# Performance work log

Measured on AMD Instinct MI355X. Metric: run time of the kernel, lower is better.

## Reference

```python
import jax, jax.numpy as jnp
import numpy as np
from jax import lax

IN_CH = 256
OUT_CH = 256
INTER = IN_CH // 2
KERNEL = 3


def setup_inputs() -> dict:
    key = jax.random.key(0)
    ks = jax.random.split(key, 6)
    B, C, H, W = 8, IN_CH, 128, 128
    x = jax.random.normal(ks[0], (B, C, H, W), dtype=jnp.float32)
    s = 1.0 / np.sqrt(C)
    Wq = jax.random.normal(ks[1], (INTER, C), dtype=jnp.float32) * s
    Wk = jax.random.normal(ks[2], (INTER, C), dtype=jnp.float32) * s
    Wv = jax.random.normal(ks[3], (INTER, C), dtype=jnp.float32) * s
    w1d = jax.random.normal(ks[4], (KERNEL,), dtype=jnp.float32) * (1.0 / np.sqrt(KERNEL))
    Wc = jax.random.normal(ks[5], (OUT_CH, INTER, 3, 3), dtype=jnp.float32) * (1.0 / np.sqrt(INTER * 9))
    return {"x": x, "Wq": Wq, "Wk": Wk, "Wv": Wv, "w1d": w1d, "Wc": Wc}


def reference(x, Wq, Wk, Wv, w1d, Wc):
    B, C, H, W = x.shape
    inter = Wq.shape[0]
    Hs, Ws = H // 4, W // 4  # 1x1 conv, stride 4, pad 0 == spatial subsample
    xs = x[:, :, ::4, ::4]  # [B, C, Hs, Ws]
    q = jnp.einsum('oc,bchw->bohw', Wq, xs).reshape(B, inter, Hs * Ws)  # [B, inter, N]
    k = jnp.einsum('oc,bchw->bohw', Wk, xs).reshape(B, inter, Hs * Ws)
    v = jnp.einsum('oc,bchw->bohw', Wv, xs).reshape(B, inter, Hs * Ws)
    # gate = softmax(Q^T K) over last dim, shape [B, N, N]
    scores = jnp.einsum('bcn,bcm->bnm', q, k)
    gate = jax.nn.softmax(scores, axis=-1)
    # gated value: [B, inter, N] -> [B, inter, Hs, Ws]
    gv = jnp.einsum('bnm,bcm->bcn', gate, v).reshape(B, inter, Hs, Ws)
    # ECA channel gating: global avg pool -> conv1d over channel dim -> sigmoid
    ca = gv.mean(axis=(2, 3))  # [B, inter]
    ca = lax.conv_general_dilated(
        ca[:, None, :],                     # [B, 1, inter]
        w1d[None, None, :],                 # [1, 1, K]
        window_strides=(1,), padding=[((KERNEL - 1) // 2,) * 2],
        dimension_numbers=('NCH', 'OIH', 'NCH'))
    ca = jax.nn.sigmoid(ca)[:, 0, :, None, None]  # [B, inter, 1, 1]
    out = gv * ca
    out = lax.conv_general_dilated(
        out, Wc, window_strides=(1, 1), padding='SAME',
        dimension_numbers=('NCHW', 'OIHW', 'NCHW'))
    return out, gate, ca
```

## Files before the change

kernel.cpp:

```cpp
#include <hip/hip_runtime.h>
#include <math.h>

#define B_   8
#define C_   256
#define CI_  128
#define N_   1024
#define HW_  32
#define CO_  256

typedef __bf16 v8bf __attribute__((ext_vector_type(8)));
typedef float  f32x4 __attribute__((ext_vector_type(4)));
typedef unsigned short ushort_t;

__device__ __forceinline__ unsigned short f2bf_rne(float f) {
    unsigned int u = __float_as_uint(f);
    unsigned int r = u + 0x7FFF + ((u >> 16) & 1);
    return (unsigned short)(r >> 16);
}
__device__ __forceinline__ float bf2f(unsigned short h) {
    return __uint_as_float(((unsigned int)h) << 16);
}
__device__ __forceinline__ v8bf ld8(const ushort_t* p) {
    return *(const v8bf*)p;
}

__global__ __launch_bounds__(256) void prep_all_kernel(
    const float* __restrict__ x,
    const float* __restrict__ Wc,
    const float* __restrict__ Wq, const float* __restrict__ Wk,
    const float* __restrict__ Wv,
    ushort_t* __restrict__ Whi, ushort_t* __restrict__ Wlo,
    ushort_t* __restrict__ Wp_hi, ushort_t* __restrict__ Wp_lo,
    ushort_t* __restrict__ xs_hi, ushort_t* __restrict__ xs_lo,
    float* __restrict__ meanb)
{
    __shared__ ushort_t lh[32 * 72];
    __shared__ ushort_t ll[32 * 72];
    const int bx = blockIdx.x;
    const int tid = threadIdx.x;

    if (bx < 1152) {
        if (bx == 0) {
            *(float4*)&meanb[tid * 4] = make_float4(0.f, 0.f, 0.f, 0.f);
        }
        int idx = bx * 256 + tid;
        int o = idx / 1152;
        int r = idx - o * 1152;
        int ci = r / 9;
        int tap = r - ci * 9;
        float v = Wc[idx];
        unsigned short h = f2bf_rne(v);
        unsigned short l = f2bf_rne(v - bf2f(h));
        int didx = o * 1152 + tap * 128 + ci;
        Whi[didx] = h; Wlo[didx] = l;
    } else if (bx < 1536) {
        int j = (bx - 1152) * 256 + tid;
        int o = j >> 8, c = j & 255;
        float v = (o < 128) ? Wq[o * 256 + c]
                : (o < 256) ? Wk[(o - 128) * 256 + c]
                            : Wv[(o - 256) * 256 + c];
        unsigned short h = f2bf_rne(v);
        unsigned short l = f2bf_rne(v - bf2f(h));
        Wp_hi[j] = h; Wp_lo[j] = l;
    } else {
        const int bx2 = bx - 1536;
        const int cq = bx2 & 3;
        const int h  = (bx2 >> 2) & 31;
        const int b  = bx2 >> 7;
        const int w = tid & 31, cg = tid >> 5;
        float v[8];
        #pragma unroll
        for (int i = 0; i < 8; ++i) {
            int c = cq * 64 + i * 8 + cg;
            v[i] = x[((size_t)(b * C_ + c) * 128 + h * 4) * 128 + w * 4];
        }
        #pragma unroll
        for (int i = 0; i < 8; ++i) {
            int cl = i * 8 + cg;
            unsigned short hi = f2bf_rne(v[i]);
            unsigned short lo = f2bf_rne(v[i] - bf2f(hi));
            lh[w * 72 + cl] = hi;
            ll[w * 72 + cl] = lo;
        }
        __syncthreads();
        const int ww = tid >> 3, cs = tid & 7;
        size_t dst = ((size_t)(b * N_) + h * 32 + ww) * 256 + cq * 64 + cs * 8;
        *(uint4*)&xs_hi[dst] = *(uint4*)&lh[ww * 72 + cs * 8];
        *(uint4*)&xs_lo[dst] = *(uint4*)&ll[ww * 72 + cs * 8];
    }
}

__global__ __launch_bounds__(256) void proj_mfma_kernel(
    const ushort_t* __restrict__ Wp_hi, const ushort_t* __restrict__ Wp_lo,
    const ushort_t* __restrict__ xs_hi, const ushort_t* __restrict__ xs_lo,
    ushort_t* __restrict__ qt_hi, ushort_t* __restrict__ qt_lo,
    ushort_t* __restrict__ kt_hi, ushort_t* __restrict__ kt_lo,
    ushort_t* __restrict__ vB_hi, ushort_t* __restrict__ vB_lo)
{
    const int lin = blockIdx.x + 16 * (blockIdx.y + 6 * blockIdx.z);
    const int b    = lin & 7;
    const int rest = lin >> 3;
    const int n0 = (rest & 15) * 64;
    const int o0 = (rest >> 4) * 64;
    const int tid = threadIdx.x;
    const int l = tid & 63, wv = tid >> 6;
    const int wy = wv >> 1, wx = wv & 1;
    const int ln = l & 15, quad = l >> 4;

    const ushort_t* Ah_p[2]; const ushort_t* Al_p[2];
    const ushort_t* Bh_p[2]; const ushort_t* Bl_p[2];
    #pragma unroll
    for (int i = 0; i < 2; ++i) {
        size_t off = (size_t)(o0 + wy * 32 + i * 16 + ln) * 256 + quad * 8;
        Ah_p[i] = Wp_hi + off; Al_p[i] = Wp_lo + off;
    }
    #pragma unroll
    for (int j = 0; j < 2; ++j) {
        size_t off = ((size_t)(b * N_) + n0 + wx * 32 + j * 16 + ln) * 256 + quad * 8;
        Bh_p[j] = xs_hi + off; Bl_p[j] = xs_lo + off;
    }

    f32x4 acc[2][2];
    #pragma unroll
    for (int i = 0; i < 2; ++i)
        #pragma unroll
        for (int j = 0; j < 2; ++j) acc[i][j] = (f32x4){0.f,0.f,0.f,0.f};

    if (o0 < 256) {
        #pragma unroll 4
        for (int k0 = 0; k0 < 256; k0 += 32) {
            v8bf Ah[2], Al[2], Bh[2], Bl[2];
            #pragma unroll
            for (int i = 0; i < 2; ++i) { Ah[i] = ld8(Ah_p[i] + k0); Al[i] = ld8(Al_p[i] + k0); }
            #pragma unroll
            for (int j = 0; j < 2; ++j) { Bh[j] = ld8(Bh_p[j] + k0); Bl[j] = ld8(Bl_p[j] + k0); }
            __builtin_amdgcn_s_setprio(1);
            #pragma unroll
            for (int i = 0; i < 2; ++i)
                #pragma unroll
                for (int j = 0; j < 2; ++j) {
                    acc[i][j] = __builtin_amdgcn_mfma_f32_16x16x32_bf16(Ah[i], Bh[j], acc[i][j], 0, 0, 0);
                    acc[i][j] = __builtin_amdgcn_mfma_f32_16x16x32_bf16(Ah[i], Bl[j], acc[i][j], 0, 0, 0);
                    acc[i][j] = __builtin_amdgcn_mfma_f32_16x16x32_bf16(Al[i], Bh[j], acc[i][j], 0, 0, 0);
                }
            __builtin_amdgcn_s_setprio(0);
        }
        ushort_t* th = (o0 < 128) ? qt_hi : kt_hi;
        ushort_t* tl = (o0 < 128) ? qt_lo : kt_lo;
        const int ob = o0 & 127;
        #pragma unroll
        for (int i = 0; i < 2; ++i)
            #pragma unroll
            for (int j = 0; j < 2; ++j) {
                int oo = ob + wy * 32 + i * 16 + quad * 4;
                int n  = n0 + wx * 32 + j * 16 + ln;
                unsigned int h01 = 0, h23 = 0, l01 = 0, l23 = 0;
                #pragma unroll
                for (int r = 0; r < 4; ++r) {
                    float f = acc[i][j][r];
                    unsigned short hh = f2bf_rne(f);
                    unsigned short lo = f2bf_rne(f - bf2f(hh));
                    if (r < 2) { h01 |= ((unsigned)hh) << (16 * r); l01 |= ((unsigned)lo) << (16 * r); }
                    else       { h23 |= ((unsigned)hh) << (16 * (r - 2)); l23 |= ((unsigned)lo) << (16 * (r - 2)); }
                }
                size_t off = ((size_t)(b * N_) + n) * 128 + oo;
                *(uint2*)&th[off] = make_uint2(h01, h23);
                *(uint2*)&tl[off] = make_uint2(l01, l23);
            }
    } else {
        #pragma unroll 4
        for (int k0 = 0; k0 < 256; k0 += 32) {
            v8bf Ah[2], Al[2], Bh[2], Bl[2];
            #pragma unroll
            for (int i = 0; i < 2; ++i) { Ah[i] = ld8(Ah_p[i] + k0); Al[i] = ld8(Al_p[i] + k0); }
            #pragma unroll
            for (int j = 0; j < 2; ++j) { Bh[j] = ld8(Bh_p[j] + k0); Bl[j] = ld8(Bl_p[j] + k0); }
            __builtin_amdgcn_s_setprio(1);
            #pragma unroll
            for (int j = 0; j < 2; ++j)
                #pragma unroll
                for (int i = 0; i < 2; ++i) {
                    acc[j][i] = __builtin_amdgcn_mfma_f32_16x16x32_bf16(Bh[j], Ah[i], acc[j][i], 0, 0, 0);
                    acc[j][i] = __builtin_amdgcn_mfma_f32_16x16x32_bf16(Bh[j], Al[i], acc[j][i], 0, 0, 0);
                    acc[j][i] = __builtin_amdgcn_mfma_f32_16x16x32_bf16(Bl[j], Ah[i], acc[j][i], 0, 0, 0);
                }
            __builtin_amdgcn_s_setprio(0);
        }
        const int mhi = (n0 >> 5) + wx;
        #pragma unroll
        for (int j = 0; j < 2; ++j)
            #pragma unroll
            for (int i = 0; i < 2; ++i) {
                int c   = (o0 - 256) + wy * 32 + i * 16 + ln;
                int mlo = j * 16 + quad * 4;
                unsigned int h01 = 0, h23 = 0, l01 = 0, l23 = 0;
                #pragma unroll
                for (int r = 0; r < 4; ++r) {
                    float f = acc[j][i][r];
                    unsigned short hh = f2bf_rne(f);
                    unsigned short lo = f2bf_rne(f - bf2f(hh));
                    if (r < 2) { h01 |= ((unsigned)hh) << (16 * r); l01 |= ((unsigned)lo) << (16 * r); }
                    else       { h23 |= ((unsigned)hh) << (16 * (r - 2)); l23 |= ((unsigned)lo) << (16 * (r - 2)); }
                }
                size_t off = (((size_t)b * 32 + mhi) * 128 + c) * 32 + mlo;
                *(uint2*)&vB_hi[off] = make_uint2(h01, h23);
                *(uint2*)&vB_lo[off] = make_uint2(l01, l23);
            }
    }
}

__global__ __launch_bounds__(512, 2) void attn_fused_kernel(
    const ushort_t* __restrict__ qt_hi, const ushort_t* __restrict__ qt_lo,
    const ushort_t* __restrict__ kt_hi, const ushort_t* __restrict__ kt_lo,
    const ushort_t* __restrict__ vB_hi, const ushort_t* __restrict__ vB_lo,
    float* __restrict__ gate, float* __restrict__ gv, float* __restrict__ meanb)
{
    __shared__ __align__(16) char gsm[65536];
    __shared__ float redA[8][32];
    __shared__ float redB[8][32];

    const int lin = blockIdx.x + 32 * blockIdx.y;
    const int b  = lin & 7;
    const int n0 = (lin >> 3) * 32;
    const int tid = threadIdx.x;
    const int l = tid & 63, w = tid >> 6;
    const int ln = l & 15, quad = l >> 4;
    const int Mw = w * 128;

    const ushort_t* qb_h = qt_hi + ((size_t)(b * N_) + n0) * 128;
    const ushort_t* qb_l = qt_lo + ((size_t)(b * N_) + n0) * 128;
    const ushort_t* kb_h = kt_hi + (size_t)(b * N_) * 128;
    const ushort_t* kb_l = kt_lo + (size_t)(b * N_) * 128;

    f32x4 acc[2][8];
    #pragma unroll
    for (int nt = 0; nt < 2; ++nt)
        #pragma unroll
        for (int mt = 0; mt < 8; ++mt) acc[nt][mt] = (f32x4){0.f,0.f,0.f,0.f};

    #pragma unroll
    for (int c0 = 0; c0 < 128; c0 += 32) {
        v8bf Ah[2], Al[2];
        #pragma unroll
        for (int nt = 0; nt < 2; ++nt) {
            size_t aoff = (size_t)(nt * 16 + ln) * 128 + c0 + quad * 8;
            Ah[nt] = ld8(qb_h + aoff); Al[nt] = ld8(qb_l + aoff);
        }
        #pragma unroll
        for (int mt = 0; mt < 8; ++mt) {
            size_t boff = (size_t)(Mw + mt * 16 + ln) * 128 + c0 + quad * 8;
            v8bf Bh = ld8(kb_h + boff);
            v8bf Bl = ld8(kb_l + boff);
            __builtin_amdgcn_s_setprio(1);
            #pragma unroll
            for (int nt = 0; nt < 2; ++nt) {
                acc[nt][mt] = __builtin_amdgcn_mfma_f32_16x16x32_bf16(Ah[nt], Bh, acc[nt][mt], 0, 0, 0);
                acc[nt][mt] = __builtin_amdgcn_mfma_f32_16x16x32_bf16(Ah[nt], Bl, acc[nt][mt], 0, 0, 0);
                acc[nt][mt] = __builtin_amdgcn_mfma_f32_16x16x32_bf16(Al[nt], Bh, acc[nt][mt], 0, 0, 0);
            }
            __builtin_amdgcn_s_setprio(0);
        }
    }

    float rmax[2][4];
    #pragma unroll
    for (int nt = 0; nt < 2; ++nt)
        #pragma unroll
        for (int r = 0; r < 4; ++r) {
            float m = acc[nt][0][r];
            #pragma unroll
            for (int mt = 1; mt < 8; ++mt) m = fmaxf(m, acc[nt][mt][r]);
            rmax[nt][r] = m;
        }
    #pragma unroll
    for (int nt = 0; nt < 2; ++nt)
        #pragma unroll
        for (int r = 0; r < 4; ++r) {
            float m = rmax[nt][r];
            #pragma unroll
            for (int xm = 1; xm <= 8; xm <<= 1) m = fmaxf(m, __shfl_xor(m, xm, 64));
            rmax[nt][r] = m;
        }
    if (ln == 0) {
        #pragma unroll
        for (int nt = 0; nt < 2; ++nt)
            #pragma unroll
            for (int r = 0; r < 4; ++r)
                redA[w][nt * 16 + quad * 4 + r] = rmax[nt][r];
    }
    __syncthreads();
    #pragma unroll
    for (int nt = 0; nt < 2; ++nt)
        #pragma unroll
        for (int r = 0; r < 4; ++r) {
            int row = nt * 16 + quad * 4 + r;
            float m0 = fmaxf(fmaxf(redA[0][row], redA[1][row]),
                             fmaxf(redA[2][row], redA[3][row]));
            float m1 = fmaxf(fmaxf(redA[4][row], redA[5][row]),
                             fmaxf(redA[6][row], redA[7][row]));
            rmax[nt][r] = fmaxf(m0, m1);
        }

    float rsum[2][4];
    #pragma unroll
    for (int nt = 0; nt < 2; ++nt)
        #pragma unroll
        for (int r = 0; r < 4; ++r) {
            float s = 0.f;
            #pragma unroll
            for (int mt = 0; mt < 8; ++mt) {
                float e = __expf(acc[nt][mt][r] - rmax[nt][r]);
                acc[nt][mt][r] = e;
                s += e;
            }
            rsum[nt][r] = s;
        }
    #pragma unroll
    for (int nt = 0; nt < 2; ++nt)
        #pragma unroll
        for (int r = 0; r < 4; ++r) {
            float s = rsum[nt][r];
            #pragma unroll
            for (int xm = 1; xm <= 8; xm <<= 1) s += __shfl_xor(s, xm, 64);
            rsum[nt][r] = s;
        }
    if (ln == 0) {
        #pragma unroll
        for (int nt = 0; nt < 2; ++nt)
            #pragma unroll
            for (int r = 0; r < 4; ++r)
                redB[w][nt * 16 + quad * 4 + r] = rsum[nt][r];
    }
    __syncthreads();
    #pragma unroll
    for (int nt = 0; nt < 2; ++nt)
        #pragma unroll
        for (int r = 0; r < 4; ++r) {
            int row = nt * 16 + quad * 4 + r;
            float inv = 1.0f / ((redB[0][row] + redB[1][row] + redB[2][row] + redB[3][row]) +
                                (redB[4][row] + redB[5][row] + redB[6][row] + redB[7][row]));
            #pragma unroll
            for (int mt = 0; mt < 8; ++mt) acc[nt][mt][r] *= inv;
        }

    #pragma unroll
    for (int nt = 0; nt < 2; ++nt)
        #pragma unroll
        for (int r = 0; r < 4; ++r) {
            int nl = nt * 16 + quad * 4 + r;
            #pragma unroll
            for (int mt = 0; mt < 8; ++mt) {
                int m = Mw + mt * 16 + ln;
                int chunk = m >> 3;
                int addr = nl * 2048 + (((chunk ^ (nl & 7))) << 4) + ((m & 7) << 1);
                *(ushort_t*)&gsm[addr] = f2bf_rne(acc[nt][mt][r]);
            }
        }
    __syncthreads();

    const ushort_t* vb_h = vB_hi + (size_t)b * CI_ * N_;
    const ushort_t* vb_l = vB_lo + (size_t)b * CI_ * N_;

    f32x4 acc2[2];
    acc2[0] = (f32x4){0.f,0.f,0.f,0.f};
    acc2[1] = (f32x4){0.f,0.f,0.f,0.f};

    #pragma unroll 4
    for (int m0 = 0; m0 < 1024; m0 += 32) {
        v8bf Bg[2];
        #pragma unroll
        for (int nt = 0; nt < 2; ++nt) {
            int nl = nt * 16 + ln;
            int chunk = (m0 >> 3) + quad;
            Bg[nt] = *(const v8bf*)&gsm[nl * 2048 + (((chunk ^ (nl & 7))) << 4)];
        }
        int c = w * 16 + ln;
        size_t aoff = (((size_t)(m0 >> 5)) * 128 + c) * 32 + quad * 8;
        v8bf Avh = ld8(vb_h + aoff);
        v8bf Avl = ld8(vb_l + aoff);
        __builtin_amdgcn_s_setprio(1);
        #pragma unroll
        for (int nt = 0; nt < 2; ++nt) {
            acc2[nt] = __builtin_amdgcn_mfma_f32_16x16x32_bf16(Avh, Bg[nt], acc2[nt], 0, 0, 0);
            acc2[nt] = __builtin_amdgcn_mfma_f32_16x16x32_bf16(Avl, Bg[nt], acc2[nt], 0, 0, 0);
        }
        __builtin_amdgcn_s_setprio(0);
    }

    #pragma unroll
    for (int nt = 0; nt < 2; ++nt) {
        int n = n0 + nt * 16 + ln;
        float4 o4 = make_float4(acc2[nt][0], acc2[nt][1], acc2[nt][2], acc2[nt][3]);
        *(float4*)&gv[((size_t)(b * N_) + n) * CI_ + w * 16 + quad * 4] = o4;
    }

    float* grow = gate + (size_t)b * N_ * N_;
    #pragma unroll
    for (int nt = 0; nt < 2; ++nt)
        #pragma unroll
        for (int r = 0; r < 4; ++r) {
            int n = n0 + nt * 16 + quad * 4 + r;
            #pragma unroll
            for (int mt = 0; mt < 8; ++mt) {
                int m = Mw + mt * 16 + ln;
                grow[(size_t)n * N_ + m] = acc[nt][mt][r];
            }
        }

    float s0 = acc2[0][0] + acc2[1][0];
    float s1 = acc2[0][1] + acc2[1][1];
    float s2 = acc2[0][2] + acc2[1][2];
    float s3 = acc2[0][3] + acc2[1][3];
    #pragma unroll
    for (int xm = 1; xm <= 8; xm <<= 1) {
        s0 += __shfl_xor(s0, xm, 64);
        s1 += __shfl_xor(s1, xm, 64);
        s2 += __shfl_xor(s2, xm, 64);
        s3 += __shfl_xor(s3, xm, 64);
    }
    if (ln == 0) {
        int cb = b * CI_ + w * 16 + quad * 4;
        atomicAdd(&meanb[cb + 0], s0);
        atomicAdd(&meanb[cb + 1], s1);
        atomicAdd(&meanb[cb + 2], s2);
        atomicAdd(&meanb[cb + 3], s3);
    }
}

__global__ __launch_bounds__(256) void gvca_prep_kernel(
    const float* __restrict__ gv, const float* __restrict__ meanb,
    const float* __restrict__ w1d,
    ushort_t* __restrict__ gvh, ushort_t* __restrict__ gvl,
    float* __restrict__ ca_out)
{
    __shared__ float ca_s[128];
    const int lin = blockIdx.x;
    const int b  = lin & 7;
    const int ns = lin >> 3;
    const int tid = threadIdx.x;

    if (tid < 128) {
        const float sc = 1.0f / 1024.0f;
        int t = b * 128 + tid;
        float left  = (tid > 0)   ? meanb[t - 1] * sc : 0.0f;
        float mid   = meanb[t] * sc;
        float right = (tid < 127) ? meanb[t + 1] * sc : 0.0f;
        float val = w1d[0] * left + w1d[1] * mid + w1d[2] * right;
        float s = 1.0f / (1.0f + __expf(-val));
        ca_s[tid] = s;
        if (ns == 0) ca_out[t] = s;
    }
    __syncthreads();

    const int cl = (tid & 31) * 4;
    const int nr = tid >> 5;
    #pragma unroll
    for (int i = 0; i < 4; ++i) {
        int n = ns * 32 + nr + i * 8;
        size_t off = ((size_t)(b * N_) + n) * 128 + cl;
        float4 v4 = *(const float4*)&gv[off];
        float vv[4] = { v4.x * ca_s[cl], v4.y * ca_s[cl + 1],
                        v4.z * ca_s[cl + 2], v4.w * ca_s[cl + 3] };
        unsigned int h01 = 0, h23 = 0, l01 = 0, l23 = 0;
        #pragma unroll
        for (int t = 0; t < 4; ++t) {
            unsigned short h = f2bf_rne(vv[t]);
            unsigned short lo = f2bf_rne(vv[t] - bf2f(h));
            if (t < 2) { h01 |= ((unsigned)h) << (16 * t); l01 |= ((unsigned)lo) << (16 * t); }
            else       { h23 |= ((unsigned)h) << (16 * (t - 2)); l23 |= ((unsigned)lo) << (16 * (t - 2)); }
        }
        *(uint2*)&gvh[off] = make_uint2(h01, h23);
        *(uint2*)&gvl[off] = make_uint2(l01, l23);
    }
}

#define BHI  0
#define BLO  17408
__global__ __launch_bounds__(256) void conv_mfma_kernel(
    const ushort_t* __restrict__ gvh, const ushort_t* __restrict__ gvl,
    const ushort_t* __restrict__ Whi, const ushort_t* __restrict__ Wlo,
    float* __restrict__ out)
{
    __shared__ __align__(16) char smem[67584];
    const int AH[2] = {34816, 51200};
    const int AL[2] = {43008, 59392};

    const int lin = blockIdx.x + 4 * (blockIdx.y + 16 * blockIdx.z);
    const int b    = lin & 7;
    const int rest = lin >> 3;
    const int o0 = (rest & 3) * 64;
    const int h0 = (rest >> 2) * 2;
    const int tid = threadIdx.x;
    const int l   = tid & 63;
    const int wv  = tid >> 6;
    const int wy  = wv >> 1;
    const int wx  = wv & 1;
    const int ln  = l & 15;
    const int quad = l >> 4;

    f32x4 acc[2][2];
    #pragma unroll
    for (int i = 0; i < 2; ++i)
        #pragma unroll
        for (int j = 0; j < 2; ++j)
            acc[i][j] = (f32x4){0.f, 0.f, 0.f, 0.f};

    const int srow0 = tid >> 3, scol = tid & 7;
    const int la0 = srow0 * 128 + scol * 16;
    const int la1 = (srow0 + 32) * 128 + scol * 16;

    for (int half = 0; half < 2; ++half) {
        __syncthreads();
        for (int u = tid; u < 136 * 8; u += 256) {
            int p  = u >> 3;
            int cs = u & 7;
            int hrel = p / 34;
            int c    = p - hrel * 34;
            int gr = h0 + hrel - 1;
            int gc = c - 1;
            bool ok = ((unsigned)gr < 32u) && ((unsigned)gc < 32u);
            uint4 h4 = make_uint4(0, 0, 0, 0), l4 = make_uint4(0, 0, 0, 0);
            if (ok) {
                size_t src = ((size_t)(b * N_) + gr * 32 + gc) * 128 + half * 64 + cs * 8;
                h4 = *(const uint4*)&gvh[src];
                l4 = *(const uint4*)&gvl[src];
            }
            int addr = p * 128 + ((cs ^ (p & 7)) << 4);
            *(uint4*)&smem[BHI + addr] = h4;
            *(uint4*)&smem[BLO + addr] = l4;
        }
        {
            int csrc0 = scol ^ (srow0 & 7);
            int csrc1 = scol ^ ((srow0 + 32) & 7);
            size_t g0 = (size_t)(o0 + srow0) * 1152 + half * 64 + csrc0 * 8;
            size_t g1 = (size_t)(o0 + srow0 + 32) * 1152 + half * 64 + csrc1 * 8;
            uint4 h0r = *(const uint4*)&Whi[g0];
            uint4 l0r = *(const uint4*)&Wlo[g0];
            uint4 h1r = *(const uint4*)&Whi[g1];
            uint4 l1r = *(const uint4*)&Wlo[g1];
            *(uint4*)&smem[AH[0] + la0] = h0r;
            *(uint4*)&smem[AL[0] + la0] = l0r;
            *(uint4*)&smem[AH[0] + la1] = h1r;
            *(uint4*)&smem[AL[0] + la1] = l1r;
        }

        for (int tap = 0; tap < 9; ++tap) {
            __syncthreads();
            uint4 nh0, nl0, nh1, nl1;
            if (tap < 8) {
                int ntap = tap + 1;
                int csrc0 = scol ^ (srow0 & 7);
                int csrc1 = scol ^ ((srow0 + 32) & 7);
                size_t g0 = (size_t)(o0 + srow0) * 1152 + ntap * 128 + half * 64 + csrc0 * 8;
                size_t g1 = (size_t)(o0 + srow0 + 32) * 1152 + ntap * 128 + half * 64 + csrc1 * 8;
                nh0 = *(const uint4*)&Whi[g0];
                nl0 = *(const uint4*)&Wlo[g0];
                nh1 = *(const uint4*)&Whi[g1];
                nl1 = *(const uint4*)&Wlo[g1];
            }
            const int ah = AH[tap & 1], al = AL[tap & 1];
            const int dy = tap / 3, dx = tap - dy * 3;
            const int pbase = (wx + dy) * 34 + dx;
            #pragma unroll
            for (int cc = 0; cc < 2; ++cc) {
                v8bf Bh[2], Bl[2], Ah2[2], Al2[2];
                #pragma unroll
                for (int j = 0; j < 2; ++j) {
                    int p = pbase + j * 16 + ln;
                    int ch = cc * 4 + quad;
                    int addr = p * 128 + ((ch ^ (p & 7)) << 4);
                    Bh[j] = *(const v8bf*)&smem[BHI + addr];
                    Bl[j] = *(const v8bf*)&smem[BLO + addr];
                }
                #pragma unroll
                for (int i = 0; i < 2; ++i) {
                    int o = wy * 32 + i * 16 + ln;
                    int ch = cc * 4 + quad;
                    int addr = o * 128 + ((ch ^ (o & 7)) << 4);
                    Ah2[i] = *(const v8bf*)&smem[ah + addr];
                    Al2[i] = *(const v8bf*)&smem[al + addr];
                }
                __builtin_amdgcn_s_setprio(1);
                #pragma unroll
                for (int i = 0; i < 2; ++i)
                    #pragma unroll
                    for (int j = 0; j < 2; ++j) {
                        acc[i][j] = __builtin_amdgcn_mfma_f32_16x16x32_bf16(Ah2[i], Bh[j], acc[i][j], 0, 0, 0);
                        acc[i][j] = __builtin_amdgcn_mfma_f32_16x16x32_bf16(Ah2[i], Bl[j], acc[i][j], 0, 0, 0);
                        acc[i][j] = __builtin_amdgcn_mfma_f32_16x16x32_bf16(Al2[i], Bh[j], acc[i][j], 0, 0, 0);
                    }
                __builtin_amdgcn_s_setprio(0);
            }
            if (tap < 8) {
                int nb = (tap + 1) & 1;
                *(uint4*)&smem[AH[nb] + la0] = nh0;
                *(uint4*)&smem[AL[nb] + la0] = nl0;
                *(uint4*)&smem[AH[nb] + la1] = nh1;
                *(uint4*)&smem[AL[nb] + la1] = nl1;
            }
        }
    }

    const int h = h0 + wx;
    #pragma unroll
    for (int i = 0; i < 2; ++i)
        #pragma unroll
        for (int j = 0; j < 2; ++j)
            #pragma unroll
            for (int r = 0; r < 4; ++r) {
                int o = o0 + wy * 32 + i * 16 + quad * 4 + r;
                int w = j * 16 + ln;
                out[(size_t)(b * CO_ + o) * N_ + h * 32 + w] = acc[i][j][r];
            }
}

extern "C" void kernel_launch(void* const* d_in, const int* in_sizes, int n_in,
                              void* d_out, int out_size, void* d_ws, size_t ws_size,
                              hipStream_t stream) {
    const float* x   = (const float*)d_in[0];
    const float* Wq  = (const float*)d_in[1];
    const float* Wk  = (const float*)d_in[2];
    const float* Wv  = (const float*)d_in[3];
    const float* w1d = (const float*)d_in[4];
    const float* Wc  = (const float*)d_in[5];

    float* out  = (float*)d_out;
    float* gate = out + 2097152;
    float* ca   = gate + 8388608;

    float*    gv      = (float*)d_ws;
    float*    meanb   = gv + 1048576;
    ushort_t* Whi     = (ushort_t*)(meanb + 1024);
    ushort_t* Wlo     = Whi + 294912;
    ushort_t* Wp_hi   = Wlo + 294912;
    ushort_t* Wp_lo   = Wp_hi + 98304;
    ushort_t* xs_hi   = Wp_lo + 98304;
    ushort_t* xs_lo   = xs_hi + 2097152;
    ushort_t* qt_hi   = xs_lo + 2097152;
    ushort_t* qt_lo   = qt_hi + 1048576;
    ushort_t* kt_hi   = qt_lo + 1048576;
    ushort_t* kt_lo   = kt_hi + 1048576;
    ushort_t* vB_hi   = kt_lo + 1048576;
    ushort_t* vB_lo   = vB_hi + 1048576;
    ushort_t* gvh     = vB_lo + 1048576;
    ushort_t* gvl     = gvh + 1048576;

    prep_all_kernel<<<dim3(2560), 256, 0, stream>>>(
        x, Wc, Wq, Wk, Wv, Whi, Wlo, Wp_hi, Wp_lo, xs_hi, xs_lo, meanb);
    proj_mfma_kernel<<<dim3(16, 6, 8), 256, 0, stream>>>(
        Wp_hi, Wp_lo, xs_hi, xs_lo, qt_hi, qt_lo, kt_hi, kt_lo, vB_hi, vB_lo);
    attn_fused_kernel<<<dim3(32, 8), 512, 0, stream>>>(
        qt_hi, qt_lo, kt_hi, kt_lo, vB_hi, vB_lo, gate, gv, meanb);
    gvca_prep_kernel<<<dim3(256), 256, 0, stream>>>(
        gv, meanb, w1d, gvh, gvl, ca);
    conv_mfma_kernel<<<dim3(4, 16, 8), 256, 0, stream>>>(
        gvh, gvl, Whi, Wlo, out);
}
```

Measured before the change: 276.0 us.

## Enlarge conv tile to four output rows with 512-thread blocks

The 3x3 conv kernel now gives each block four output rows instead of two, using 8 waves and 512 threads. The halo tile in LDS grows from 4 to 6 rows, which cuts the relative halo overhead. Each weight tap slice is now loaded once per block for twice as many outputs. The block count halves to 256 and the kernel needs about 85KB of dynamic shared memory, with one block per CU via launch bounds. Separately, the x subsample load is rewritten with float4-based indexing that reads only the .x component.

```diff
diff --git a/kernel.cpp b/kernel.cpp
--- a/kernel.cpp
+++ b/kernel.cpp
@@ -68,11 +68,12 @@
         const int h  = (bx2 >> 2) & 31;
         const int b  = bx2 >> 7;
         const int w = tid & 31, cg = tid >> 5;
+        const float4* xrow = (const float4*)x;
         float v[8];
         #pragma unroll
         for (int i = 0; i < 8; ++i) {
             int c = cq * 64 + i * 8 + cg;
-            v[i] = x[((size_t)(b * C_ + c) * 128 + h * 4) * 128 + w * 4];
+            v[i] = xrow[(size_t)(b * C_ + c) * 4096 + h * 128 + w].x;
         }
         #pragma unroll
         for (int i = 0; i < 8; ++i) {
@@ -474,27 +475,27 @@
     }
 }
 
-#define BHI  0
-#define BLO  17408
-__global__ __launch_bounds__(256) void conv_mfma_kernel(
+#define CV_BHI  0
+#define CV_BLO  26112
+__global__ __launch_bounds__(512, 1) void conv_mfma_kernel(
     const ushort_t* __restrict__ gvh, const ushort_t* __restrict__ gvl,
     const ushort_t* __restrict__ Whi, const ushort_t* __restrict__ Wlo,
     float* __restrict__ out)
 {
-    __shared__ __align__(16) char smem[67584];
-    const int AH[2] = {34816, 51200};
-    const int AL[2] = {43008, 59392};
-
-    const int lin = blockIdx.x + 4 * (blockIdx.y + 16 * blockIdx.z);
+    extern __shared__ __align__(16) char smem[];
+    const int AH[2] = {52224, 68608};
+    const int AL[2] = {60416, 76800};
+
+    const int lin = blockIdx.x;
     const int b    = lin & 7;
     const int rest = lin >> 3;
     const int o0 = (rest & 3) * 64;
-    const int h0 = (rest >> 2) * 2;
+    const int h0 = (rest >> 2) * 4;
     const int tid = threadIdx.x;
     const int l   = tid & 63;
     const int wv  = tid >> 6;
-    const int wy  = wv >> 1;
-    const int wx  = wv & 1;
+    const int wy  = wv >> 2;
+    const int wx  = wv & 3;
     const int ln  = l & 15;
     const int quad = l >> 4;
 
@@ -505,13 +506,13 @@
         for (int j = 0; j < 2; ++j)
             acc[i][j] = (f32x4){0.f, 0.f, 0.f, 0.f};
 
-    const int srow0 = tid >> 3, scol = tid & 7;
-    const int la0 = srow0 * 128 + scol * 16;
-    const int la1 = (srow0 + 32) * 128 + scol * 16;
+    const int srow = tid >> 3, scol = tid & 7;
+    const int la   = srow * 128 + scol * 16;
+    const int csrc = scol ^ (srow & 7);
 
     for (int half = 0; half < 2; ++half) {
         __syncthreads();
-        for (int u = tid; u < 136 * 8; u += 256) {
+        for (int u = tid; u < 204 * 8; u += 512) {
             int p  = u >> 3;
             int cs = u & 7;
             int hrel = p / 34;
@@ -526,37 +527,22 @@
                 l4 = *(const uint4*)&gvl[src];
             }
             int addr = p * 128 + ((cs ^ (p & 7)) << 4);
-            *(uint4*)&smem[BHI + addr] = h4;
-            *(uint4*)&smem[BLO + addr] = l4;
+            *(uint4*)&smem[CV_BHI + addr] = h4;
+            *(uint4*)&smem[CV_BLO + addr] = l4;
         }
         {
-            int csrc0 = scol ^ (srow0 & 7);
-            int csrc1 = scol ^ ((srow0 + 32) & 7);
-            size_t g0 = (size_t)(o0 + srow0) * 1152 + half * 64 + csrc0 * 8;
-            size_t g1 = (size_t)(o0 + srow0 + 32) * 1152 + half * 64 + csrc1 * 8;
-            uint4 h0r = *(const uint4*)&Whi[g0];
-            uint4 l0r = *(const uint4*)&Wlo[g0];
-            uint4 h1r = *(const uint4*)&Whi[g1];
-            uint4 l1r = *(const uint4*)&Wlo[g1];
-            *(uint4*)&smem[AH[0] + la0] = h0r;
-            *(uint4*)&smem[AL[0] + la0] = l0r;
-            *(uint4*)&smem[AH[0] + la1] = h1r;
-            *(uint4*)&smem[AL[0] + la1] = l1r;
+            size_t g = (size_t)(o0 + srow) * 1152 + half * 64 + csrc * 8;
+            *(uint4*)&smem[AH[0] + la] = *(const uint4*)&Whi[g];
+            *(uint4*)&smem[AL[0] + la] = *(const uint4*)&Wlo[g];
         }
 
         for (int tap = 0; tap < 9; ++tap) {
             __syncthreads();
-            uint4 nh0, nl0, nh1, nl1;
+            uint4 nh, nl;
             if (tap < 8) {
-                int ntap = tap + 1;
-                int csrc0 = scol ^ (srow0 & 7);
-                int csrc1 = scol ^ ((srow0 + 32) & 7);
-                size_t g0 = (size_t)(o0 + srow0) * 1152 + ntap * 128 + half * 64 + csrc0 * 8;
-                size_t g1 = (size_t)(o0 + srow0 + 32) * 1152 + ntap * 128 + half * 64 + csrc1 * 8;
-                nh0 = *(const uint4*)&Whi[g0];
-                nl0 = *(const uint4*)&Wlo[g0];
-                nh1 = *(const uint4*)&Whi[g1];
-                nl1 = *(const uint4*)&Wlo[g1];
+                size_t g = (size_t)(o0 + srow) * 1152 + (tap + 1) * 128 + half * 64 + csrc * 8;
+                nh = *(const uint4*)&Whi[g];
+                nl = *(const uint4*)&Wlo[g];
             }
             const int ah = AH[tap & 1], al = AL[tap & 1];
             const int dy = tap / 3, dx = tap - dy * 3;
@@ -569,8 +555,8 @@
                     int p = pbase + j * 16 + ln;
                     int ch = cc * 4 + quad;
                     int addr = p * 128 + ((ch ^ (p & 7)) << 4);
-                    Bh[j] = *(const v8bf*)&smem[BHI + addr];
-                    Bl[j] = *(const v8bf*)&smem[BLO + addr];
+                    Bh[j] = *(const v8bf*)&smem[CV_BHI + addr];
+                    Bl[j] = *(const v8bf*)&smem[CV_BLO + addr];
                 }
                 #pragma unroll
                 for (int i = 0; i < 2; ++i) {
@@ -593,10 +579,8 @@
             }
             if (tap < 8) {
                 int nb = (tap + 1) & 1;
-                *(uint4*)&smem[AH[nb] + la0] = nh0;
-                *(uint4*)&smem[AL[nb] + la0] = nl0;
-                *(uint4*)&smem[AH[nb] + la1] = nh1;
-                *(uint4*)&smem[AL[nb] + la1] = nl1;
+                *(uint4*)&smem[AH[nb] + la] = nh;
+                *(uint4*)&smem[AL[nb] + la] = nl;
             }
         }
     }
@@ -645,6 +629,13 @@
     ushort_t* gvh     = vB_lo + 1048576;
     ushort_t* gvl     = gvh + 1048576;
 
+    static bool s_attr_done = false;
+    if (!s_attr_done) {
+        hipFuncSetAttribute((const void*)conv_mfma_kernel,
+                            hipFuncAttributeMaxDynamicSharedMemorySize, 84992);
+        s_attr_done = true;
+    }
+
     prep_all_kernel<<<dim3(2560), 256, 0, stream>>>(
         x, Wc, Wq, Wk, Wv, Whi, Wlo, Wp_hi, Wp_lo, xs_hi, xs_lo, meanb);
     proj_mfma_kernel<<<dim3(16, 6, 8), 256, 0, stream>>>(
@@ -653,6 +644,6 @@
         qt_hi, qt_lo, kt_hi, kt_lo, vB_hi, vB_lo, gate, gv, meanb);
     gvca_prep_kernel<<<dim3(256), 256, 0, stream>>>(
         gv, meanb, w1d, gvh, gvl, ca);
-    conv_mfma_kernel<<<dim3(4, 16, 8), 256, 0, stream>>>(
+    conv_mfma_kernel<<<dim3(256), 512, 84992, stream>>>(
         gvh, gvl, Whi, Wlo, out);
 }
```

Measured after the change: 276.5 us, median of 2. No clear change (+0.2%).
